# Performance work log

Measured on AMD Instinct MI355X. Metric: run time of the kernel, lower is better.

The kernel has to match this reference:

```python
import jax, jax.numpy as jnp
import numpy as np
import math

# ---- config (mirrors FastRCNNRoIHeads init args) ----
B, N, C = 8, 2048, 2            # images, proposals/img, classes (incl. background)
K = 100                          # detections_per_img
IMG_H, IMG_W = 512, 512
SCORE_THRESH = 0.05
NMS_THRESH = 0.4
MIN_SIZE = 0.01
WX, WY, WW, WH = 10.0, 10.0, 5.0, 5.0   # BoxCoder weights
BBOX_XFORM_CLIP = math.log(1000.0 / 16.0)


def setup_inputs() -> dict:
    key = jax.random.key(0)
    k1, k2, k3, k4, k5 = jax.random.split(key, 5)
    prop_clss = jax.random.normal(k1, (B, N, C), dtype=jnp.float32)
    prop_regs = 0.1 * jax.random.normal(k2, (B, N, 4), dtype=jnp.float32)
    prop_qlts = jax.random.normal(k3, (B, N, 1), dtype=jnp.float32)
    # valid proposal boxes inside the image: x1,y1 in [0,448), w,h in [16,128)
    xy1 = jax.random.uniform(k4, (B, N, 2), dtype=jnp.float32) * 380.0
    wh = 16.0 + jax.random.uniform(k5, (B, N, 2), dtype=jnp.float32) * 112.0
    props = jnp.concatenate([xy1, xy1 + wh], axis=-1)
    return {"prop_clss": prop_clss, "prop_regs": prop_regs,
            "prop_qlts": prop_qlts, "props": props}


def _decode(regs, props):
    # torchvision BoxCoder.decode_single, class-agnostic [N,4] deltas
    w = props[:, 2] - props[:, 0]
    h = props[:, 3] - props[:, 1]
    cx = props[:, 0] + 0.5 * w
    cy = props[:, 1] + 0.5 * h
    dx, dy = regs[:, 0] / WX, regs[:, 1] / WY
    dw = jnp.minimum(regs[:, 2] / WW, BBOX_XFORM_CLIP)
    dh = jnp.minimum(regs[:, 3] / WH, BBOX_XFORM_CLIP)
    pcx, pcy = dx * w + cx, dy * h + cy
    pw, ph = jnp.exp(dw) * w, jnp.exp(dh) * h
    return jnp.stack([pcx - 0.5 * pw, pcy - 0.5 * ph,
                      pcx + 0.5 * pw, pcy + 0.5 * ph], axis=-1)


def _iou_matrix(b):
    area = (b[:, 2] - b[:, 0]) * (b[:, 3] - b[:, 1])
    lt = jnp.maximum(b[:, None, :2], b[None, :, :2])
    rb = jnp.minimum(b[:, None, 2:], b[None, :, 2:])
    wh = jnp.clip(rb - lt, 0.0)
    inter = wh[..., 0] * wh[..., 1]
    return inter / (area[:, None] + area[None, :] - inter + 1e-9)


def _postprocess_one(clss, regs, qlts, props):
    boxes = _decode(regs, props)
    boxes = jnp.stack([jnp.clip(boxes[:, 0], 0.0, IMG_W),
                       jnp.clip(boxes[:, 1], 0.0, IMG_H),
                       jnp.clip(boxes[:, 2], 0.0, IMG_W),
                       jnp.clip(boxes[:, 3], 0.0, IMG_H)], axis=-1)
    small_ok = ((boxes[:, 2] - boxes[:, 0]) >= MIN_SIZE) & \
               ((boxes[:, 3] - boxes[:, 1]) >= MIN_SIZE)
    raw = jax.nn.softmax(clss, axis=-1)[:, 1:]          # [N, C-1]
    q = jax.nn.sigmoid(qlts[:, 0])                      # [N]
    scores = (q[:, None] * raw).reshape(-1)             # [N*(C-1)]
    raw_f = raw.reshape(-1)
    Cm1 = C - 1
    M = N * Cm1
    prop_idx = jnp.arange(M) // Cm1
    cls_idx = jnp.arange(M) % Cm1 + 1
    valid = (raw_f > SCORE_THRESH) & small_ok[prop_idx]
    cand_boxes = boxes[prop_idx]                        # [M,4]
    # batched_nms: offset boxes per class so NMS runs per class
    max_coord = jnp.max(cand_boxes)
    boxes_off = cand_boxes + (cls_idx.astype(boxes.dtype) * (max_coord + 1.0))[:, None]
    masked = jnp.where(valid, scores, -1.0)
    order = jnp.argsort(-masked)
    b_s = cand_boxes[order]
    bo_s = boxes_off[order]
    s_s = scores[order]
    c_s = cls_idx[order]
    v_s = valid[order]
    iou = _iou_matrix(bo_s)                             # [M,M]
    idxs = jnp.arange(M)

    def step(keep, i):
        sup = (iou[i] > NMS_THRESH) & (idxs > i)
        keep = jnp.where(keep[i], keep & ~sup, keep)
        return keep, None

    keep, _ = jax.lax.scan(step, v_s, idxs)
    rank = jnp.cumsum(keep.astype(jnp.int32)) - 1
    dest = jnp.where(keep & (rank < K), rank, K)        # K = dump slot
    out_b = jnp.zeros((K + 1, 4), boxes.dtype).at[dest].set(b_s)[:K]
    out_s = jnp.zeros((K + 1,), boxes.dtype).at[dest].set(s_s)[:K]
    out_c = jnp.zeros((K + 1,), jnp.int32).at[dest].set(c_s.astype(jnp.int32))[:K]
    return out_b, out_s, out_c


def reference(prop_clss, prop_regs, prop_qlts, props):
    boxes, scores, classes = jax.vmap(_postprocess_one)(
        prop_clss, prop_regs, prop_qlts, props)
    return boxes, scores, classes
```

## Files before the change

kernel.cpp:

```cpp
#include <hip/hip_runtime.h>
#include <stdint.h>

#define NPROP 2048
#define NCLS  2
#define KDET  100
#define BT    512
#define NMS_TH 0.4f

__device__ __forceinline__ float dec_score(uint64_t k) {
    uint32_t u = ~(uint32_t)(k >> 32);
    uint32_t bits = (u & 0x80000000u) ? (u & 0x7FFFFFFFu) : ~u;
    return __uint_as_float(bits);
}

__device__ __forceinline__ float bcastf(float v, int srclane) {
    return __uint_as_float((uint32_t)__builtin_amdgcn_readlane(__float_as_int(v), srclane));
}

__device__ __forceinline__ float iou5(float ax1, float ay1, float ax2, float ay2, float aa,
                                      float bx1, float by1, float bx2, float by2, float ba) {
    float ltx = fmaxf(ax1, bx1), lty = fmaxf(ay1, by1);
    float rbx = fminf(ax2, bx2), rby = fminf(ay2, by2);
    float iw = fmaxf(__fsub_rn(rbx, ltx), 0.0f);
    float ih = fmaxf(__fsub_rn(rby, lty), 0.0f);
    float inter = __fmul_rn(iw, ih);
    float denom = __fadd_rn(__fsub_rn(__fadd_rn(aa, ba), inter), 1e-9f);
    return __fdiv_rn(inter, denom);
}

__device__ __forceinline__ void decode_one(
    const float* __restrict__ clss, const float* __restrict__ regs,
    const float* __restrict__ qlts, const float* __restrict__ props,
    int b, int i, float4& boxOut, uint64_t& keyOut, float& mxOut)
{
    const float CLIPV = 4.135166556742356f;
    float4 p  = ((const float4*)props)[b * NPROP + i];
    float4 rg = ((const float4*)regs)[b * NPROP + i];
    float2 cc = ((const float2*)clss)[b * NPROP + i];
    float  qv = qlts[(size_t)b * NPROP + i];

    float w  = __fsub_rn(p.z, p.x);
    float h  = __fsub_rn(p.w, p.y);
    float cx = __fadd_rn(p.x, __fmul_rn(0.5f, w));
    float cy = __fadd_rn(p.y, __fmul_rn(0.5f, h));
    float dx = __fdiv_rn(rg.x, 10.0f);
    float dy = __fdiv_rn(rg.y, 10.0f);
    float dw = fminf(__fdiv_rn(rg.z, 5.0f), CLIPV);
    float dh = fminf(__fdiv_rn(rg.w, 5.0f), CLIPV);
    float pcx = __fadd_rn(__fmul_rn(dx, w), cx);
    float pcy = __fadd_rn(__fmul_rn(dy, h), cy);
    float pw  = __fmul_rn(expf(dw), w);
    float ph  = __fmul_rn(expf(dh), h);
    float x1 = __fsub_rn(pcx, __fmul_rn(0.5f, pw));
    float y1 = __fsub_rn(pcy, __fmul_rn(0.5f, ph));
    float x2 = __fadd_rn(pcx, __fmul_rn(0.5f, pw));
    float y2 = __fadd_rn(pcy, __fmul_rn(0.5f, ph));
    x1 = fminf(fmaxf(x1, 0.0f), 512.0f);
    y1 = fminf(fmaxf(y1, 0.0f), 512.0f);
    x2 = fminf(fmaxf(x2, 0.0f), 512.0f);
    y2 = fminf(fmaxf(y2, 0.0f), 512.0f);
    bool small_ok = (__fsub_rn(x2, x1) >= 0.01f) && (__fsub_rn(y2, y1) >= 0.01f);

    float m  = fmaxf(cc.x, cc.y);
    float e0 = expf(__fsub_rn(cc.x, m));
    float e1 = expf(__fsub_rn(cc.y, m));
    float raw = __fdiv_rn(e1, __fadd_rn(e0, e1));
    float sq  = __fdiv_rn(1.0f, __fadd_rn(1.0f, expf(-qv)));
    float score = __fmul_rn(sq, raw);
    bool valid = (raw > 0.05f) && small_ok;
    float masked = valid ? score : -1.0f;

    boxOut = make_float4(x1, y1, x2, y2);
    uint32_t fb = __float_as_uint(masked);
    uint32_t u  = (fb & 0x80000000u) ? ~fb : (fb | 0x80000000u);
    keyOut = ((uint64_t)(~u) << 32) | (uint32_t)i;
    mxOut = fmaxf(fmaxf(x1, y1), fmaxf(x2, y2));
}

__device__ __forceinline__ void bitonic2048(uint64_t key[4], uint64_t* skey,
                                            int idxBase, int lane)
{
    for (int k = 2; k <= NPROP; k <<= 1) {
        for (int j = k >> 1; j > 0; j >>= 1) {
            if (j >= 256) {
                __syncthreads();
#pragma unroll
                for (int r = 0; r < 4; ++r) {
                    int idx = idxBase + r;
                    skey[(idx >> 2) | ((idx & 3) << 9)] = key[r];
                }
                __syncthreads();
#pragma unroll
                for (int r = 0; r < 4; ++r) {
                    int idx  = idxBase + r;
                    int pidx = idx ^ j;
                    uint64_t o = skey[(pidx >> 2) | ((pidx & 3) << 9)];
                    bool takeMin = (((idx & k) == 0) == ((idx & j) == 0));
                    bool lt = key[r] < o;
                    uint64_t mn = lt ? key[r] : o, mx = lt ? o : key[r];
                    key[r] = takeMin ? mn : mx;
                }
            } else if (j >= 4) {
                int lx = j >> 2;
#pragma unroll
                for (int r = 0; r < 4; ++r) {
                    int idx = idxBase + r;
                    uint64_t o = __shfl_xor(key[r], lx, 64);
                    bool takeMin = (((idx & k) == 0) == ((lane & lx) == 0));
                    bool lt = key[r] < o;
                    uint64_t mn = lt ? key[r] : o, mx = lt ? o : key[r];
                    key[r] = takeMin ? mn : mx;
                }
            } else {
#pragma unroll
                for (int r = 0; r < 4; ++r) {
                    if ((r & j) == 0) {
                        int rh = r | j;
                        int idx = idxBase + r;
                        bool up = ((idx & k) == 0);
                        uint64_t a = key[r], c2 = key[rh];
                        bool lt = a < c2;
                        uint64_t mn = lt ? a : c2, mx = lt ? c2 : a;
                        key[r] = up ? mn : mx; key[rh] = up ? mx : mn;
                    }
                }
            }
        }
    }
}

template<int ELEMS, int EPL>
__device__ __forceinline__ void wavesortN(uint64_t* buf, int lane)
{
    uint64_t q[EPL];
#pragma unroll
    for (int r = 0; r < EPL; ++r) q[r] = buf[lane * EPL + r];
    for (int k2 = 2; k2 <= ELEMS; k2 <<= 1) {
        for (int j = k2 >> 1; j > 0; j >>= 1) {
            if (j >= EPL) {
                int lx = j / EPL;
#pragma unroll
                for (int r = 0; r < EPL; ++r) {
                    int idx = lane * EPL + r;
                    uint64_t o = __shfl_xor(q[r], lx, 64);
                    bool takeMin = (((idx & k2) == 0) == ((idx & j) == 0));
                    bool lt = q[r] < o;
                    uint64_t mn = lt ? q[r] : o, mx = lt ? o : q[r];
                    q[r] = takeMin ? mn : mx;
                }
            } else {
#pragma unroll
                for (int r = 0; r < EPL; ++r) {
                    if ((r & j) == 0) {
                        int rh = r | j;
                        int idx = lane * EPL + r;
                        bool up = ((idx & k2) == 0);
                        uint64_t a = q[r], c2 = q[rh];
                        bool lt = a < c2;
                        uint64_t mn = lt ? a : c2, mx = lt ? c2 : a;
                        q[r] = up ? mn : mx; q[rh] = up ? mx : mn;
                    }
                }
            }
        }
    }
#pragma unroll
    for (int r = 0; r < EPL; ++r) buf[lane * EPL + r] = q[r];
}

__device__ __forceinline__ int phaseC2(
    const uint64_t* keys, int nv, const float4* sboxp, float off,
    uint64_t* s_cp1, uint64_t* s_cpX, uint64_t* s_cp2,
    uint64_t* s_in1, uint64_t* s_in2,
    float4* s_kbox, float* s_karea, int* s_keep, int* s_kept, int lane, int wv)
{
    int c = 0;
    while (true) {
        __syncthreads();
        int kept = *s_kept;
        if (c >= nv || kept >= KDET) break;
        int W  = nv - c;
        int W1 = W < 64 ? W : 64;
        int W2 = (W > 64) ? ((W - 64) < 64 ? (W - 64) : 64) : 0;
        bool have1 = lane < W1, have2 = lane < W2;

        float ax1=0.f, ay1=0.f, ax2=0.f, ay2=0.f, aa=0.f;
        float bx1=0.f, by1=0.f, bx2=0.f, by2=0.f, ba=0.f;
        if (have1) {
            float4 bx = sboxp[(uint32_t)keys[c + lane]];
            ax1 = __fadd_rn(bx.x, off); ay1 = __fadd_rn(bx.y, off);
            ax2 = __fadd_rn(bx.z, off); ay2 = __fadd_rn(bx.w, off);
            aa  = __fmul_rn(__fsub_rn(ax2, ax1), __fsub_rn(ay2, ay1));
        }
        if (have2) {
            float4 bx = sboxp[(uint32_t)keys[c + 64 + lane]];
            bx1 = __fadd_rn(bx.x, off); by1 = __fadd_rn(bx.y, off);
            bx2 = __fadd_rn(bx.z, off); by2 = __fadd_rn(bx.w, off);
            ba  = __fmul_rn(__fsub_rn(bx2, bx1), __fsub_rn(by2, by1));
        }

        uint64_t cp1 = 0, cpX = 0, cp2 = 0;
#pragma unroll
        for (int t = 0; t < 8; ++t) {
            int i = wv + (t << 3);
            {
                bool rowok = (i < W1);
                int isrc = rowok ? i : 0;
                float rx1 = bcastf(ax1, isrc), ry1 = bcastf(ay1, isrc);
                float rx2 = bcastf(ax2, isrc), ry2 = bcastf(ay2, isrc);
                float ra  = bcastf(aa , isrc);
                bool p1 = rowok && have1 && (lane > i) &&
                          (iou5(rx1,ry1,rx2,ry2,ra, ax1,ay1,ax2,ay2,aa) > NMS_TH);
                uint64_t bm1 = (uint64_t)__ballot(p1);
                cp1 |= ((bm1 >> lane) & 1ull) << isrc;
                bool px = rowok && have2 &&
                          (iou5(rx1,ry1,rx2,ry2,ra, bx1,by1,bx2,by2,ba) > NMS_TH);
                uint64_t bmx = (uint64_t)__ballot(px);
                cpX |= ((bmx >> lane) & 1ull) << isrc;
            }
            {
                bool rowok = (i < W2);
                int isrc = rowok ? i : 0;
                float rx1 = bcastf(bx1, isrc), ry1 = bcastf(by1, isrc);
                float rx2 = bcastf(bx2, isrc), ry2 = bcastf(by2, isrc);
                float ra  = bcastf(ba , isrc);
                bool p2 = rowok && have2 && (lane > i) &&
                          (iou5(rx1,ry1,rx2,ry2,ra, bx1,by1,bx2,by2,ba) > NMS_TH);
                uint64_t bm2 = (uint64_t)__ballot(p2);
                cp2 |= ((bm2 >> lane) & 1ull) << isrc;
            }
        }
        s_cp1[(wv << 6) | lane] = cp1;
        s_cpX[(wv << 6) | lane] = cpX;
        s_cp2[(wv << 6) | lane] = cp2;

        bool si1 = false, si2 = false;
        if (kept) {
            for (int ki = wv; ki < kept; ki += 8) {
                float4 ko = s_kbox[ki];
                float  ka = s_karea[ki];
                si1 = si1 || (have1 && iou5(ko.x,ko.y,ko.z,ko.w,ka, ax1,ay1,ax2,ay2,aa) > NMS_TH);
                si2 = si2 || (have2 && iou5(ko.x,ko.y,ko.z,ko.w,ka, bx1,by1,bx2,by2,ba) > NMS_TH);
            }
        }
        uint64_t i1b = (uint64_t)__ballot(si1);
        uint64_t i2b = (uint64_t)__ballot(si2);
        if (lane == 0) { s_in1[wv] = i1b; s_in2[wv] = i2b; }
        __syncthreads();

        if (wv == 0) {
            uint64_t col1 = 0, colX = 0, col2 = 0, in1 = 0, in2 = 0;
#pragma unroll
            for (int w2i = 0; w2i < 8; ++w2i) {
                col1 |= s_cp1[(w2i << 6) | lane];
                colX |= s_cpX[(w2i << 6) | lane];
                col2 |= s_cp2[(w2i << 6) | lane];
                in1  |= s_in1[w2i];
                in2  |= s_in2[w2i];
            }
            uint64_t below = ~(~0ull << lane);

            bool alive1 = have1 && !((in1 >> lane) & 1ull);
            uint64_t keepM1 = (uint64_t)__ballot(alive1);
            for (int it = 0; it < 64; ++it) {
                uint64_t nk = (uint64_t)__ballot(alive1 && ((col1 & keepM1) == 0ull));
                if (nk == keepM1) break;
                keepM1 = nk;
            }
            int quota = KDET - kept;
            int n1 = __popcll(keepM1);
            int take1 = n1 < quota ? n1 : quota;
            int rank1 = __popcll(keepM1 & below);
            if ((((keepM1 >> lane) & 1ull) != 0ull) && rank1 < quota) {
                s_keep[kept + rank1]  = c + lane;
                s_kbox[kept + rank1]  = make_float4(ax1, ay1, ax2, ay2);
                s_karea[kept + rank1] = aa;
            }
            int kept1 = kept + take1;
            int take2 = 0;
            if (kept1 < KDET && W2 > 0) {
                bool alive2 = have2 && !((in2 >> lane) & 1ull) && ((colX & keepM1) == 0ull);
                uint64_t keepM2 = (uint64_t)__ballot(alive2);
                for (int it = 0; it < 64; ++it) {
                    uint64_t nk = (uint64_t)__ballot(alive2 && ((col2 & keepM2) == 0ull));
                    if (nk == keepM2) break;
                    keepM2 = nk;
                }
                int quota2 = KDET - kept1;
                int n2 = __popcll(keepM2);
                take2 = n2 < quota2 ? n2 : quota2;
                int rank2 = __popcll(keepM2 & below);
                if ((((keepM2 >> lane) & 1ull) != 0ull) && rank2 < quota2) {
                    s_keep[kept1 + rank2]  = c + 64 + lane;
                    s_kbox[kept1 + rank2]  = make_float4(bx1, by1, bx2, by2);
                    s_karea[kept1 + rank2] = ba;
                }
            }
            if (lane == 0) *s_kept = kept1 + take2;
        }
        c += 128;
    }
    __syncthreads();
    return *s_kept;
}

__global__ __launch_bounds__(BT) void PRISM_71511205479155_kernel(
    const float* __restrict__ clss, const float* __restrict__ regs,
    const float* __restrict__ qlts, const float* __restrict__ props,
    float* __restrict__ out, int B)
{
    __shared__ float4   sbox[NPROP];
    __shared__ __align__(16) char s_reg1[16384];
    __shared__ uint64_t s_cp1[512];
    __shared__ uint64_t s_cpX[512];
    __shared__ uint64_t s_cp2[512];
    __shared__ uint64_t s_in1[8], s_in2[8];
    __shared__ float4   s_kbox[KDET];
    __shared__ float    s_karea[KDET];
    __shared__ int      s_keep[KDET];
    __shared__ int      s_wsum[8];
    __shared__ int      s_maxc, s_kept, s_beta, s_M, s_totV, s_fb;

    uint32_t* hist = (uint32_t*)s_reg1;
    uint64_t* cand = (uint64_t*)(s_reg1 + 2048);
    uint64_t* skey = (uint64_t*)s_reg1;

    const int b = blockIdx.x, tid = threadIdx.x, lane = tid & 63, wv = tid >> 6;
    const int idxBase = (wv << 8) | (lane << 2);

    hist[tid & 511] = 0;
    if (tid == 0) { s_maxc = 0; s_kept = 0; s_beta = -1; s_M = 0; s_totV = 0; s_fb = 0; }
    __syncthreads();

    uint64_t key[4];
    float thmax = 0.0f;
#pragma unroll
    for (int r = 0; r < 4; ++r) {
        int i = idxBase + r;
        float4 bx; uint64_t k; float mx;
        decode_one(clss, regs, qlts, props, b, i, bx, k, mx);
        sbox[i] = bx; key[r] = k;
        thmax = fmaxf(thmax, mx);
        uint32_t bkt = (uint32_t)(k >> 53);
        if (bkt < 1024)
            atomicAdd(&hist[bkt >> 1], (bkt & 1) ? 0x10000u : 1u);
    }
#pragma unroll
    for (int d = 1; d < 64; d <<= 1) thmax = fmaxf(thmax, __shfl_xor(thmax, d, 64));
    if (lane == 0) atomicMax(&s_maxc, __float_as_int(thmax));
    __syncthreads();

    {
        uint32_t wword = hist[tid & 511];
        uint32_t c0 = wword & 0xFFFFu, c1 = wword >> 16;
        uint32_t local = c0 + c1;
        uint32_t incl = local;
#pragma unroll
        for (int d = 1; d < 64; d <<= 1) {
            uint32_t v = __shfl_up(incl, d, 64);
            if (lane >= d) incl += v;
        }
        if (lane == 63) s_wsum[wv] = (int)incl;
        __syncthreads();
        int base = 0, tot = 0;
#pragma unroll
        for (int w = 0; w < 8; ++w) {
            int sv = s_wsum[w];
            tot += sv;
            if (w < wv) base += sv;
        }
        int target = tot < 192 ? tot : 192;
        uint32_t run = (uint32_t)base + incl - local;
        uint32_t cc2[2] = {c0, c1};
#pragma unroll
        for (int r = 0; r < 2; ++r) {
            uint32_t ci = run + cc2[r];
            if (target > 0 && (int)run < target && (int)ci >= target) {
                s_beta = 2 * tid + r;
                s_M = (int)ci;
                if (ci > 512) s_fb = 1;
            }
            run = ci;
        }
        if (tid == 0) s_totV = tot;
        __syncthreads();
    }

    const float off = __fadd_rn(__int_as_float(s_maxc), 1.0f);
    const int beta = s_beta, M = s_M, totV = s_totV;
    int fb = s_fb;

    if (!fb && M > 0) {
        bool pr[4]; uint64_t bal[4]; int wcnt[4];
#pragma unroll
        for (int r = 0; r < 4; ++r) {
            pr[r]  = ((int)(key[r] >> 53) <= beta);
            bal[r] = (uint64_t)__ballot(pr[r]);
            wcnt[r] = __popcll(bal[r]);
        }
        int wtot = wcnt[0] + wcnt[1] + wcnt[2] + wcnt[3];
        if (lane == 0) s_wsum[wv] = wtot;
        __syncthreads();
        int base2 = 0;
#pragma unroll
        for (int w = 0; w < 8; ++w) if (w < wv) base2 += s_wsum[w];
        uint64_t below = ~(~0ull << lane);
        int roff = 0;
#pragma unroll
        for (int r = 0; r < 4; ++r) {
            if (pr[r]) {
                int pos = base2 + roff + __popcll(bal[r] & below);
                cand[pos] = key[r];
            }
            roff += wcnt[r];
        }
        int sortN = (M <= 256) ? 256 : 512;
        for (int t = M + tid; t < sortN; t += BT) cand[t] = ~0ull;
        __syncthreads();

        if (wv == 0) {
            if (sortN == 256) wavesortN<256, 4>(cand, lane);
            else              wavesortN<512, 8>(cand, lane);
        }
        __syncthreads();
    }

    int kept = 0;
    if (!fb && M > 0)
        kept = phaseC2(cand, M, sbox, off, s_cp1, s_cpX, s_cp2, s_in1, s_in2,
                       s_kbox, s_karea, s_keep, &s_kept, lane, wv);

    bool needFull = fb || (kept < KDET && M < totV);
    if (needFull) {
        if (tid == 0) s_kept = 0;
        bitonic2048(key, skey, idxBase, lane);
        __syncthreads();
#pragma unroll
        for (int r = 0; r < 4; ++r) skey[idxBase + r] = key[r];
        kept = phaseC2(skey, totV, sbox, off, s_cp1, s_cpX, s_cp2, s_in1, s_in2,
                       s_kbox, s_karea, s_keep, &s_kept, lane, wv);
    }
    const uint64_t* fkeys = needFull ? skey : cand;

    float* out_boxes  = out;
    float* out_scores = out + (size_t)B * KDET * 4;
    float* out_cls    = out + (size_t)B * KDET * 5;
    for (int s = tid; s < KDET; s += BT) {
        float* ob = out_boxes + ((size_t)b * KDET + s) * 4;
        if (s < kept) {
            uint64_t kk = fkeys[s_keep[s]];
            float4 bx = sbox[(uint32_t)kk];
            ob[0] = bx.x; ob[1] = bx.y; ob[2] = bx.z; ob[3] = bx.w;
            out_scores[(size_t)b * KDET + s] = dec_score(kk);
            out_cls[(size_t)b * KDET + s]    = 1.0f;
        } else {
            ob[0] = 0.0f; ob[1] = 0.0f; ob[2] = 0.0f; ob[3] = 0.0f;
            out_scores[(size_t)b * KDET + s] = 0.0f;
            out_cls[(size_t)b * KDET + s]    = 0.0f;
        }
    }
}

extern "C" void kernel_launch(void* const* d_in, const int* in_sizes, int n_in,
                              void* d_out, int out_size, void* d_ws, size_t ws_size,
                              hipStream_t stream) {
    const float* clss  = (const float*)d_in[0];
    const float* regs  = (const float*)d_in[1];
    const float* qlts  = (const float*)d_in[2];
    const float* props = (const float*)d_in[3];
    float* out = (float*)d_out;

    int B = in_sizes[0] / (NPROP * NCLS);

    PRISM_71511205479155_kernel<<<B, BT, 0, stream>>>(clss, regs, qlts, props, out, B);
}
```

Measured before the change: 33.86 us.

## Add one-shot bitmask NMS path for candidate sets up to 256

When the candidate count is at most 256, all eight waves build the full suppression bitmask matrix, one ballot per IoU row, and merge it into shared memory with atomicOr. A single wave then runs a fixed-point iteration over the keep masks in place of the sequential phaseC2 greedy loop. The three scratch arrays now alias one shared region that also holds the column masks. The aim is to replace the serial dependency chain with parallel IoU work. The cost is that every pair is computed, the iteration count can reach 256, and correctness depends on the fixed point matching greedy NMS.

```diff
diff --git a/kernel.cpp b/kernel.cpp
--- a/kernel.cpp
+++ b/kernel.cpp
@@ -311,9 +311,7 @@
 {
     __shared__ float4   sbox[NPROP];
     __shared__ __align__(16) char s_reg1[16384];
-    __shared__ uint64_t s_cp1[512];
-    __shared__ uint64_t s_cpX[512];
-    __shared__ uint64_t s_cp2[512];
+    __shared__ __align__(16) char s_reg2[12288];
     __shared__ uint64_t s_in1[8], s_in2[8];
     __shared__ float4   s_kbox[KDET];
     __shared__ float    s_karea[KDET];
@@ -324,6 +322,10 @@
     uint32_t* hist = (uint32_t*)s_reg1;
     uint64_t* cand = (uint64_t*)(s_reg1 + 2048);
     uint64_t* skey = (uint64_t*)s_reg1;
+    uint64_t* s_cp1 = (uint64_t*)s_reg2;
+    uint64_t* s_cpX = (uint64_t*)(s_reg2 + 4096);
+    uint64_t* s_cp2 = (uint64_t*)(s_reg2 + 8192);
+    uint64_t* s_col = (uint64_t*)s_reg2;
 
     const int b = blockIdx.x, tid = threadIdx.x, lane = tid & 63, wv = tid >> 6;
     const int idxBase = (wv << 8) | (lane << 2);
@@ -389,6 +391,7 @@
     const float off = __fadd_rn(__int_as_float(s_maxc), 1.0f);
     const int beta = s_beta, M = s_M, totV = s_totV;
     int fb = s_fb;
+    bool oneshot = (!fb && M > 0 && M <= 256);
 
     if (!fb && M > 0) {
         bool pr[4]; uint64_t bal[4]; int wcnt[4];
@@ -416,6 +419,7 @@
         }
         int sortN = (M <= 256) ? 256 : 512;
         for (int t = M + tid; t < sortN; t += BT) cand[t] = ~0ull;
+        if (oneshot) { s_col[tid] = 0; s_col[tid + 512] = 0; }
         __syncthreads();
 
         if (wv == 0) {
@@ -426,12 +430,110 @@
     }
 
     int kept = 0;
-    if (!fb && M > 0)
+    if (oneshot) {
+        float qx1[4], qy1[4], qx2[4], qy2[4], qa[4];
+        bool  qv[4];
+#pragma unroll
+        for (int w = 0; w < 4; ++w) {
+            int j = (w << 6) | lane;
+            qv[w] = (j < M);
+            qx1[w] = qy1[w] = qx2[w] = qy2[w] = qa[w] = 0.f;
+            if (qv[w]) {
+                float4 bx = sbox[(uint32_t)cand[j]];
+                qx1[w] = __fadd_rn(bx.x, off); qy1[w] = __fadd_rn(bx.y, off);
+                qx2[w] = __fadd_rn(bx.z, off); qy2[w] = __fadd_rn(bx.w, off);
+                qa[w]  = __fmul_rn(__fsub_rn(qx2[w], qx1[w]), __fsub_rn(qy2[w], qy1[w]));
+            }
+        }
+
+        uint64_t colM[4][4] = {{0,0,0,0},{0,0,0,0},{0,0,0,0},{0,0,0,0}};
+        const int nW = (M + 63) >> 6;
+#pragma unroll
+        for (int wr = 0; wr < 4; ++wr) {
+            if (wr < nW) {
+#pragma unroll
+                for (int t = 0; t < 8; ++t) {
+                    int il = wv + (t << 3);
+                    int gi = (wr << 6) | il;
+                    bool rowok = (gi < M);
+                    float rx1 = bcastf(qx1[wr], il), ry1 = bcastf(qy1[wr], il);
+                    float rx2 = bcastf(qx2[wr], il), ry2 = bcastf(qy2[wr], il);
+                    float ra  = bcastf(qa[wr],  il);
+#pragma unroll
+                    for (int w = 0; w < 4; ++w) {
+                        if (w >= wr) {
+                            int gj = (w << 6) | lane;
+                            bool pred = rowok && qv[w] && (gj > gi) &&
+                                (iou5(rx1,ry1,rx2,ry2,ra,
+                                      qx1[w],qy1[w],qx2[w],qy2[w],qa[w]) > NMS_TH);
+                            uint64_t bm = (uint64_t)__ballot(pred);
+                            colM[w][wr] |= ((bm >> lane) & 1ull) << il;
+                        }
+                    }
+                }
+            }
+        }
+#pragma unroll
+        for (int w = 0; w < 4; ++w) {
+#pragma unroll
+            for (int wr = 0; wr < 4; ++wr) {
+                if (colM[w][wr])
+                    atomicOr((unsigned long long*)&s_col[((((w << 6) | lane)) << 2) | wr],
+                             (unsigned long long)colM[w][wr]);
+            }
+        }
+        __syncthreads();
+
+        if (wv == 0) {
+            uint64_t cR[4][4];
+#pragma unroll
+            for (int w = 0; w < 4; ++w)
+#pragma unroll
+                for (int wr = 0; wr < 4; ++wr)
+                    cR[w][wr] = s_col[((((w << 6) | lane)) << 2) | wr];
+
+            bool alive[4]; uint64_t K[4];
+#pragma unroll
+            for (int w = 0; w < 4; ++w) {
+                alive[w] = (((w << 6) | lane) < M);
+                K[w] = (uint64_t)__ballot(alive[w]);
+            }
+            for (int it = 0; it < 256; ++it) {
+                bool p0 = alive[0] && (((cR[0][0]&K[0])|(cR[0][1]&K[1])|(cR[0][2]&K[2])|(cR[0][3]&K[3])) == 0ull);
+                bool p1 = alive[1] && (((cR[1][0]&K[0])|(cR[1][1]&K[1])|(cR[1][2]&K[2])|(cR[1][3]&K[3])) == 0ull);
+                bool p2 = alive[2] && (((cR[2][0]&K[0])|(cR[2][1]&K[1])|(cR[2][2]&K[2])|(cR[2][3]&K[3])) == 0ull);
+                bool p3 = alive[3] && (((cR[3][0]&K[0])|(cR[3][1]&K[1])|(cR[3][2]&K[2])|(cR[3][3]&K[3])) == 0ull);
+                uint64_t n0 = (uint64_t)__ballot(p0);
+                uint64_t n1 = (uint64_t)__ballot(p1);
+                uint64_t n2 = (uint64_t)__ballot(p2);
+                uint64_t n3 = (uint64_t)__ballot(p3);
+                bool same = (n0 == K[0]) && (n1 == K[1]) && (n2 == K[2]) && (n3 == K[3]);
+                K[0] = n0; K[1] = n1; K[2] = n2; K[3] = n3;
+                if (same) break;
+            }
+            int t0 = __popcll(K[0]), t1 = __popcll(K[1]), t2 = __popcll(K[2]), t3 = __popcll(K[3]);
+            int total = t0 + t1 + t2 + t3;
+            uint64_t below = ~(~0ull << lane);
+            int bases[4] = {0, t0, t0 + t1, t0 + t1 + t2};
+#pragma unroll
+            for (int w = 0; w < 4; ++w) {
+                if ((K[w] >> lane) & 1ull) {
+                    int rank = bases[w] + __popcll(K[w] & below);
+                    if (rank < KDET) s_keep[rank] = (w << 6) | lane;
+                }
+            }
+            if (lane == 0) s_kept = total < KDET ? total : KDET;
+        }
+        __syncthreads();
+        kept = s_kept;
+    } else if (!fb && M > 0) {
         kept = phaseC2(cand, M, sbox, off, s_cp1, s_cpX, s_cp2, s_in1, s_in2,
                        s_kbox, s_karea, s_keep, &s_kept, lane, wv);
+    }
 
     bool needFull = fb || (kept < KDET && M < totV);
     if (needFull) {
+        __syncthreads();
         if (tid == 0) s_kept = 0;
         bitonic2048(key, skey, idxBase, lane);
         __syncthreads();
```

After: 34.92 us. +3.1%, slower.
